# Performance work log

Measured on AMD Instinct MI355X. Metric: run time of the kernel, lower is better.

Reference implementation:

```python
import jax, jax.numpy as jnp
from jax import lax
import numpy as np

B = 16
H0 = 56
W0 = 56
C = 768
HEADS = 12
SCALES = 3
WS = 7
LC = C // SCALES          # 256 local channels per scale group
HD = C // HEADS           # 64 head dim (= conv groups)
LH = HEADS // SCALES      # 4 local heads per group


def setup_inputs() -> dict:
    key = jax.random.key(0)
    ks = jax.random.split(key, 6)
    x = jax.random.normal(ks[0], (B, H0 * W0, C), jnp.float32)
    w_qkv = jax.random.normal(ks[1], (3 * C, C), jnp.float32) * 0.02
    w_proj = jax.random.normal(ks[2], (C, C), jnp.float32) * 0.02
    b_proj = jnp.zeros((C,), jnp.float32)
    # grouped conv (groups = head_dim = 64): weight (out=LC, in_per_group=LC//HD, 3, 3)
    conv1_w = jax.random.normal(ks[3], (LC, LC // HD, 3, 3), jnp.float32) * 0.05
    conv1_b = jnp.zeros((LC,), jnp.float32)
    conv2_w = jax.random.normal(ks[4], (LC, LC // HD, 3, 3), jnp.float32) * 0.05
    conv2_b = jnp.zeros((LC,), jnp.float32)
    return {"x": x, "w_qkv": w_qkv, "w_proj": w_proj, "b_proj": b_proj,
            "conv1_w": conv1_w, "conv1_b": conv1_b,
            "conv2_w": conv2_w, "conv2_b": conv2_b,
            "H": H0, "W": W0}


def _grouped_conv(xc, w, b, stride, pad, dil):
    y = lax.conv_general_dilated(
        xc, w, window_strides=(stride, stride),
        padding=((pad, pad), (pad, pad)), rhs_dilation=(dil, dil),
        feature_group_count=HD,
        dimension_numbers=("NCHW", "OIHW", "NCHW"))
    return y + b[None, :, None, None]


def _maxpool2(xc):
    return lax.reduce_window(xc, -jnp.inf, lax.max,
                             (1, 1, 2, 2), (1, 1, 2, 2), "VALID")


def _patchify(arr):
    # arr: (B, LC, Hs, Ws) -> (B*n_region, LH, WS*WS, HD)
    b, lc, hs, ws = arr.shape
    a = arr.reshape(b, lc, hs // WS, WS, ws // WS, WS)
    a = a.transpose(0, 2, 4, 3, 5, 1).reshape(-1, WS * WS, lc)
    a = a.reshape(-1, WS * WS, LH, lc // LH).transpose(0, 2, 1, 3)
    return a


def reference(x, w_qkv, w_proj, b_proj, conv1_w, conv1_b, conv2_w, conv2_b, H, W):
    scale = HD ** -0.5
    Bx, N, Cx = x.shape
    # (B, N, 3C) -> (B, H, W, 3, C) -> (B, 3, C, H, W)
    qkv = (x @ w_qkv.T).reshape(Bx, H, W, 3, Cx).transpose(0, 3, 4, 1, 2)
    N_g = (H // WS) * (W // WS)
    conv_params = [(conv1_w, conv1_b, 1, 1, 1), (conv2_w, conv2_b, 2, 2, 2)]
    outs = []
    for i in range(SCALES):
        g = qkv[:, :, i * LC:(i + 1) * LC]  # (B, 3, LC, H, W)
        Hs, Ws = H >> i, W >> i
        if i > 0:
            w, b, st, pd, dl = conv_params[i - 1]
            g = g.reshape(Bx * 3, LC, H, W)
            g = _maxpool2(_grouped_conv(g, w, b, st, pd, dl))
            g = g.reshape(Bx, 3, LC, Hs, Ws)
        q = _patchify(g[:, 0])
        k = _patchify(g[:, 1])
        v = _patchify(g[:, 2])
        attn = jax.nn.softmax(jnp.einsum("whpd,whqd->whpq", q, k) * scale, axis=-1)
        y = jnp.einsum("whpq,whqd->whpd", attn, v)  # (B*nreg, LH, 49, HD)
        nreg = (Hs // WS) * (Ws // WS)
        y = y.reshape(Bx, nreg, LH, WS * WS, HD).transpose(0, 2, 1, 3, 4)
        if i > 0:
            y = jnp.tile(y, (1, 1, N_g // nreg, 1, 1))
        outs.append(y)
    fused = jnp.concatenate(outs, axis=1)  # (B, HEADS, N_g, 49, HD)
    fused = fused.reshape(Bx, HEADS, -1, HD).transpose(0, 2, 1, 3).reshape(Bx, N, Cx)
    return fused @ w_proj.T + b_proj
```

## Files before the change

kernel.cpp:

```cpp
#include <hip/hip_runtime.h>

typedef __attribute__((ext_vector_type(4))) float f32x4;
typedef __attribute__((ext_vector_type(8))) short bf16x8;
typedef __attribute__((ext_vector_type(4))) unsigned short u16x4;
typedef unsigned short u16;

__device__ static u16   g_xh[(size_t)50176 * 768];
__device__ static u16   g_wqkvh[(size_t)2304 * 768];
__device__ static u16   g_wprojh[(size_t)768 * 768];
__device__ static u16   g_qkv[(size_t)50176 * 2304];
__device__ static u16   g_g1[(size_t)48 * 784 * 256];
__device__ static u16   g_g2[(size_t)48 * 196 * 256];
__device__ static u16   g_fh[(size_t)50176 * 768];

static __device__ __forceinline__ u16 f2bf(float x){
  unsigned u = __float_as_uint(x);
  u += 0x7fffu + ((u >> 16) & 1u);
  return (u16)(u >> 16);
}
static __device__ __forceinline__ float bf2f(u16 h){
  return __uint_as_float(((unsigned)h) << 16);
}

__global__ __launch_bounds__(256)
void cvt_bf16_3(const float* __restrict__ i0, u16* __restrict__ o0, int n0,
                const float* __restrict__ i1, u16* __restrict__ o1, int n1,
                const float* __restrict__ i2, u16* __restrict__ o2, int n2)
{
  const int total = n0 + n1 + n2;
  int i = blockIdx.x * blockDim.x + threadIdx.x;
  const int stride = gridDim.x * blockDim.x;
  for (; i < total; i += stride) {
    const float* in; u16* out; int j = i;
    if (j < n0)           { in = i0; out = o0; }
    else if (j < n0 + n1) { in = i1; out = o1; j -= n0; }
    else                  { in = i2; out = o2; j -= n0 + n1; }
    const f32x4 v = ((const f32x4*)in)[j];
    u16x4 o;
    #pragma unroll
    for (int k = 0; k < 4; k++) o[k] = f2bf(v[k]);
    ((u16x4*)out)[j] = o;
  }
}

template<bool BIAS, typename OUT_T>
__global__ __launch_bounds__(512, 2)
void gemm256(const u16* __restrict__ A0, const u16* __restrict__ Bw,
             const float* __restrict__ bias, OUT_T* __restrict__ C,
             int N, int K, int GX)
{
  __shared__ __align__(16) char ldsb[4 * 32768];
  const int tid = threadIdx.x;
  const int lane = tid & 63;
  const int w = tid >> 6;
  const int wm = w >> 2;
  const int wn = w & 3;
  const int l15 = lane & 15, l4 = lane >> 4;

  const int nwg = gridDim.x;
  const int bid = blockIdx.x;
  const int q8 = nwg >> 3, r8 = nwg & 7;
  const int xcd = bid & 7, lid = bid >> 3;
  const int swz = (xcd < r8 ? xcd * (q8 + 1) : r8 * (q8 + 1) + (xcd - r8) * q8) + lid;
  const int bn = swz % GX;
  const int bm = swz / GX;

  const int sq = tid >> 3;
  const int sp = tid & 7;
  const int tt = sp ^ (sq & 7);
  const int sa = tt >> 2, scc = tt & 3;
  const int srow0 = sq * 2 + sa;
  const u16* a0 = A0 + (size_t)(bm * 256 + srow0) * K + scc * 8;
  const u16* a1 = A0 + (size_t)(bm * 256 + 128 + srow0) * K + scc * 8;
  const u16* b0 = Bw + (size_t)(bn * 256 + srow0) * K + scc * 8;
  const u16* b1 = Bw + (size_t)(bn * 256 + 128 + srow0) * K + scc * 8;
  const int wofs = w << 10;

  #define GLDS(srcp, ldsoff) __builtin_amdgcn_global_load_lds( \
      (__attribute__((address_space(1))) const void*)(srcp),   \
      (__attribute__((address_space(3))) void*)(ldsb + (ldsoff)), 16, 0, 0)

  auto STAGE = [&](int s) {
    const int bb = (s & 3) << 15;
    const int ko = s * 32;
    GLDS(a0 + ko, bb + wofs);
    GLDS(a1 + ko, bb + 8192 + wofs);
    GLDS(b0 + ko, bb + 16384 + wofs);
    GLDS(b1 + ko, bb + 24576 + wofs);
  };

  f32x4 acc[8][4];
  #pragma unroll
  for (int i = 0; i < 8; i++)
    #pragma unroll
    for (int j = 0; j < 4; j++) acc[i][j] = (f32x4)0.f;

  auto COMPUTE = [&](int t) {
    const char* base = ldsb + ((t & 3) << 15);
    bf16x8 bfr[4], afr[8];
    #pragma unroll
    for (int ni = 0; ni < 4; ni++) {
      const int r = wn * 64 + ni * 16 + l15;
      const int pr = r >> 1;
      const int p = (((r & 1) << 2) + l4) ^ (pr & 7);
      bfr[ni] = *(const bf16x8*)(base + 16384 + pr * 128 + p * 16);
    }
    #pragma unroll
    for (int mi = 0; mi < 8; mi++) {
      const int r = wm * 128 + mi * 16 + l15;
      const int pr = r >> 1;
      const int p = (((r & 1) << 2) + l4) ^ (pr & 7);
      afr[mi] = *(const bf16x8*)(base + pr * 128 + p * 16);
    }
    __builtin_amdgcn_s_setprio(1);
    #pragma unroll
    for (int mi = 0; mi < 8; mi++)
      #pragma unroll
      for (int ni = 0; ni < 4; ni++)
        acc[mi][ni] = __builtin_amdgcn_mfma_f32_16x16x32_bf16(afr[mi], bfr[ni], acc[mi][ni], 0, 0, 0);
    __builtin_amdgcn_s_setprio(0);
  };

  const int T = K >> 5;
  STAGE(0);
  STAGE(1);
  for (int t = 0; t < T - 2; ++t) {
    STAGE(t + 2);
    asm volatile("s_waitcnt vmcnt(8)" ::: "memory");
    __builtin_amdgcn_sched_barrier(0);
    __builtin_amdgcn_s_barrier();
    __builtin_amdgcn_sched_barrier(0);
    COMPUTE(t);
  }
  asm volatile("s_waitcnt vmcnt(4)" ::: "memory");
  __builtin_amdgcn_sched_barrier(0);
  __builtin_amdgcn_s_barrier();
  __builtin_amdgcn_sched_barrier(0);
  COMPUTE(T - 2);
  asm volatile("s_waitcnt vmcnt(0)" ::: "memory");
  __builtin_amdgcn_sched_barrier(0);
  __builtin_amdgcn_s_barrier();
  __builtin_amdgcn_sched_barrier(0);
  COMPUTE(T - 1);
  #undef GLDS

  #pragma unroll
  for (int mi = 0; mi < 8; mi++)
    #pragma unroll
    for (int ni = 0; ni < 4; ni++) {
      const int col = bn * 256 + wn * 64 + ni * 16 + l15;
      const float bv = BIAS ? bias[col] : 0.f;
      #pragma unroll
      for (int reg = 0; reg < 4; reg++) {
        const int row = bm * 256 + wm * 128 + mi * 16 + (l4 << 2) + reg;
        const float val = acc[mi][ni][reg] + bv;
        if constexpr (sizeof(OUT_T) == 2) C[(size_t)row * N + col] = (OUT_T)f2bf(val);
        else                              C[(size_t)row * N + col] = val;
      }
    }
}

__global__ __launch_bounds__(256)
void conv_all(const u16* __restrict__ qkv,
              const float* __restrict__ c1w, const float* __restrict__ c1b,
              u16* __restrict__ g1,
              const float* __restrict__ c2w, const float* __restrict__ c2b,
              u16* __restrict__ g2)
{
  __shared__ float wl[64 * 145];
  const int g = threadIdx.x;
  const int ty = threadIdx.y;
  const int tid = ty * 64 + g;
  const int bt = blockIdx.x;
  const int b = bt / 3, t = bt - b * 3;
  const bool is1 = blockIdx.y < 196;

  const float* wsrc = is1 ? c1w : c2w;
  for (int i = tid; i < 9216; i += 256) {
    const int oc = i / 36, rem = i - oc * 36;
    wl[(oc >> 2) * 145 + (oc & 3) * 36 + rem] = wsrc[i];
  }
  __syncthreads();
  const float* wg = &wl[g * 145];

  if (is1) {
    const int p = blockIdx.y * 4 + ty;
    const int y = p / 28, x = p - y * 28;

    f32x4 f[4][4];
    #pragma unroll
    for (int i = 0; i < 4; i++) {
      const int iy = 2 * y - 1 + i;
      #pragma unroll
      for (int k = 0; k < 4; k++) {
        const int ix = 2 * x - 1 + k;
        f32x4 v = (f32x4)0.f;
        if (iy >= 0 && iy < 56 && ix >= 0 && ix < 56) {
          const u16x4 in4 = *(const u16x4*)&qkv[(size_t)(b * 3136 + iy * 56 + ix) * 2304 + t * 768 + 256 + g * 4];
          v[0] = bf2f(in4[0]); v[1] = bf2f(in4[1]); v[2] = bf2f(in4[2]); v[3] = bf2f(in4[3]);
        }
        f[i][k] = v;
      }
    }

    const f32x4 bias4 = *(const f32x4*)&c1b[g * 4];
    f32x4 best;
    #pragma unroll
    for (int j = 0; j < 4; j++) best[j] = -3.4e38f;

    #pragma unroll
    for (int dy = 0; dy < 2; dy++)
      #pragma unroll
      for (int dx = 0; dx < 2; dx++) {
        f32x4 c4 = bias4;
        #pragma unroll
        for (int ky = 0; ky < 3; ky++)
          #pragma unroll
          for (int kx = 0; kx < 3; kx++) {
            const f32x4 in4 = f[dy + ky][dx + kx];
            #pragma unroll
            for (int oc = 0; oc < 4; oc++) {
              const float* wp = &wg[oc * 36 + ky * 3 + kx];
              c4[oc] += in4[0] * wp[0] + in4[1] * wp[9] + in4[2] * wp[18] + in4[3] * wp[27];
            }
          }
        #pragma unroll
        for (int j = 0; j < 4; j++) best[j] = fmaxf(best[j], c4[j]);
      }
    u16x4 o4;
    #pragma unroll
    for (int j = 0; j < 4; j++) o4[j] = f2bf(best[j]);
    *(u16x4*)&g1[((size_t)bt * 784 + p) * 256 + g * 4] = o4;
  } else {
    const int p = (blockIdx.y - 196) * 4 + ty;
    const int y = p / 14, x = p - y * 14;

    const f32x4 bias4 = *(const f32x4*)&c2b[g * 4];
    f32x4 best;
    #pragma unroll
    for (int j = 0; j < 4; j++) best[j] = -3.4e38f;

    #pragma unroll
    for (int dy = 0; dy < 2; dy++)
      #pragma unroll
      for (int dx = 0; dx < 2; dx++) {
        const int py = 2 * y + dy, px = 2 * x + dx;
        f32x4 c4 = bias4;
        #pragma unroll
        for (int ky = 0; ky < 3; ky++) {
          const int iy = py * 2 - 2 + ky * 2;
          if (iy < 0 || iy >= 56) continue;
          #pragma unroll
          for (int kx = 0; kx < 3; kx++) {
            const int ix = px * 2 - 2 + kx * 2;
            if (ix < 0 || ix >= 56) continue;
            const u16x4 in4 = *(const u16x4*)&qkv[(size_t)(b * 3136 + iy * 56 + ix) * 2304 + t * 768 + 512 + g * 4];
            const float f0 = bf2f(in4[0]), f1 = bf2f(in4[1]), f2 = bf2f(in4[2]), f3 = bf2f(in4[3]);
            #pragma unroll
            for (int oc = 0; oc < 4; oc++) {
              const float* wp = &wg[oc * 36 + ky * 3 + kx];
              c4[oc] += f0 * wp[0] + f1 * wp[9] + f2 * wp[18] + f3 * wp[27];
            }
          }
        }
        #pragma unroll
        for (int j = 0; j < 4; j++) best[j] = fmaxf(best[j], c4[j]);
      }
    u16x4 o4;
    #pragma unroll
    for (int j = 0; j < 4; j++) o4[j] = f2bf(best[j]);
    *(u16x4*)&g2[((size_t)bt * 196 + p) * 256 + g * 4] = o4;
  }
}

template<int SRC>
static __device__ __forceinline__
void attn_body(const u16* __restrict__ src, u16* __restrict__ fh,
               int side, int Hs, int head_base, int rep,
               int unit, int lane, char* vb, char* pb)
{
  const int nreg = side * side;
  const int h = unit & 3; unit >>= 2;
  const int r = unit % nreg;
  const int b = unit / nreg;
  const int hr = r / side, wr = r - hr * side;
  const int l15 = lane & 15, l4 = lane >> 4;

  auto gidx = [&](int t, int pp, int c) -> size_t {
    const int py = pp / 7, px = pp - py * 7;
    const int yy = hr * 7 + py, xx = wr * 7 + px;
    if (SRC == 0) return ((size_t)(b * 3136 + yy * 56 + xx)) * 2304 + (size_t)(t * 768 + h * 64 + c);
    else          return ((size_t)(b * 3 + t)) * ((size_t)Hs * Hs * 256) + (size_t)(yy * Hs + xx) * 256 + h * 64 + c;
  };

  for (int i = lane; i < 1024; i += 64) {
    const int q = i >> 4, dc = i & 15;
    const int qs = q > 48 ? 48 : q;
    const u16x4 v4 = *(const u16x4*)&src[gidx(2, qs, dc * 4)];
    *(u16x4*)(vb + ((q * 128 + dc * 8) ^ (((q >> 3) & 3) << 5))) = v4;
  }

  f32x4 s[4][4];
  #pragma unroll
  for (int i = 0; i < 4; i++)
    #pragma unroll
    for (int j = 0; j < 4; j++) s[i][j] = (f32x4)0.f;

  bf16x8 bk[4][2];
  #pragma unroll
  for (int ni = 0; ni < 4; ni++) {
    const int q = ni * 16 + l15;
    const int qs = q > 48 ? 48 : q;
    #pragma unroll
    for (int ks = 0; ks < 2; ks++)
      bk[ni][ks] = *(const bf16x8*)&src[gidx(1, qs, ks * 32 + l4 * 8)];
  }
  #pragma unroll
  for (int mi = 0; mi < 4; mi++) {
    const int p = mi * 16 + l15;
    const int ps = p > 48 ? 48 : p;
    const bf16x8 a0 = *(const bf16x8*)&src[gidx(0, ps, l4 * 8)];
    const bf16x8 a1 = *(const bf16x8*)&src[gidx(0, ps, 32 + l4 * 8)];
    #pragma unroll
    for (int ni = 0; ni < 4; ni++) {
      s[mi][ni] = __builtin_amdgcn_mfma_f32_16x16x32_bf16(a0, bk[ni][0], s[mi][ni], 0, 0, 0);
      s[mi][ni] = __builtin_amdgcn_mfma_f32_16x16x32_bf16(a1, bk[ni][1], s[mi][ni], 0, 0, 0);
    }
  }

  #pragma unroll
  for (int ni = 0; ni < 4; ni++) {
    const bool bad = (ni * 16 + l15) > 48;
    #pragma unroll
    for (int mi = 0; mi < 4; mi++)
      #pragma unroll
      for (int reg = 0; reg < 4; reg++)
        s[mi][ni][reg] = bad ? -1e30f : s[mi][ni][reg];
  }

  float inv[4][4];
  #pragma unroll
  for (int mi = 0; mi < 4; mi++)
    #pragma unroll
    for (int reg = 0; reg < 4; reg++) {
      float m = fmaxf(fmaxf(s[mi][0][reg], s[mi][1][reg]), fmaxf(s[mi][2][reg], s[mi][3][reg]));
      m = fmaxf(m, __shfl_xor(m, 1));
      m = fmaxf(m, __shfl_xor(m, 2));
      m = fmaxf(m, __shfl_xor(m, 4));
      m = fmaxf(m, __shfl_xor(m, 8));
      float partial = 0.f;
      #pragma unroll
      for (int ni = 0; ni < 4; ni++) {
        const float e = __expf((s[mi][ni][reg] - m) * 0.125f);
        s[mi][ni][reg] = e;
        partial += e;
      }
      partial += __shfl_xor(partial, 1);
      partial += __shfl_xor(partial, 2);
      partial += __shfl_xor(partial, 4);
      partial += __shfl_xor(partial, 8);
      inv[mi][reg] = 1.f / partial;
    }

  #pragma unroll
  for (int mi = 0; mi < 4; mi++)
    #pragma unroll
    for (int ni = 0; ni < 4; ni++)
      #pragma unroll
      for (int reg = 0; reg < 4; reg++) {
        const int row = mi * 16 + l4 * 4 + reg;
        const int col = ni * 16 + l15;
        *(u16*)(pb + ((row * 128 + col * 2) ^ ((row & 7) << 4))) = f2bf(s[mi][ni][reg]);
      }
  __syncthreads();

  f32x4 o[4][4];
  #pragma unroll
  for (int i = 0; i < 4; i++)
    #pragma unroll
    for (int j = 0; j < 4; j++) o[i][j] = (f32x4)0.f;

  #pragma unroll
  for (int ks = 0; ks < 2; ks++) {
    bf16x8 bv[4];
    #pragma unroll
    for (int ni = 0; ni < 4; ni++)
      #pragma unroll
      for (int j = 0; j < 8; j++) {
        const int q = ks * 32 + l4 * 8 + j;
        bv[ni][j] = *(const short*)(vb + ((q * 128 + (ni * 16 + l15) * 2) ^ (((q >> 3) & 3) << 5)));
      }
    #pragma unroll
    for (int mi = 0; mi < 4; mi++) {
      const int row = mi * 16 + l15;
      const bf16x8 pa = *(const bf16x8*)(pb + ((row * 128 + (ks * 4 + l4) * 16) ^ ((row & 7) << 4)));
      #pragma unroll
      for (int ni = 0; ni < 4; ni++)
        o[mi][ni] = __builtin_amdgcn_mfma_f32_16x16x32_bf16(pa, bv[ni], o[mi][ni], 0, 0, 0);
    }
  }

  const int head = head_base + h;
  #pragma unroll
  for (int mi = 0; mi < 4; mi++)
    #pragma unroll
    for (int reg = 0; reg < 4; reg++) {
      const int p = mi * 16 + l4 * 4 + reg;
      if (p >= 49) continue;
      const float iv = inv[mi][reg];
      u16 hv[4];
      #pragma unroll
      for (int ni = 0; ni < 4; ni++) hv[ni] = f2bf(o[mi][ni][reg] * iv);
      for (int m = 0; m < rep; m++) {
        const size_t ob = ((size_t)b * 3136 + (size_t)(m * nreg + r) * 49 + p) * 768 + head * 64 + l15;
        #pragma unroll
        for (int ni = 0; ni < 4; ni++) fh[ob + ni * 16] = hv[ni];
      }
    }
}

__global__ __launch_bounds__(256)
void attn_all(const u16* __restrict__ qkv, const u16* __restrict__ g1,
              const u16* __restrict__ g2, u16* __restrict__ fh)
{
  __shared__ __align__(16) u16 sV[4][64 * 64];
  __shared__ __align__(16) u16 sP[4][64 * 64];
  const int tid = threadIdx.x;
  const int lane = tid & 63;
  const int w = tid >> 6;
  char* vb = (char*)sV[w];
  char* pb = (char*)sP[w];
  const int bid = blockIdx.x;

  if (bid < 1024) {
    attn_body<0>(qkv, fh, 8, 56, 0, 1,  bid * 4 + w,          lane, vb, pb);
  } else if (bid < 1280) {
    attn_body<1>(g1,  fh, 4, 28, 4, 4,  (bid - 1024) * 4 + w, lane, vb, pb);
  } else {
    attn_body<1>(g2,  fh, 2, 14, 8, 16, (bid - 1280) * 4 + w, lane, vb, pb);
  }
}

extern "C" void kernel_launch(void* const* d_in, const int* in_sizes, int n_in,
                              void* d_out, int out_size, void* d_ws, size_t ws_size,
                              hipStream_t stream)
{
  const float* x      = (const float*)d_in[0];
  const float* w_qkv  = (const float*)d_in[1];
  const float* w_proj = (const float*)d_in[2];
  const float* b_proj = (const float*)d_in[3];
  const float* c1w    = (const float*)d_in[4];
  const float* c1b    = (const float*)d_in[5];
  const float* c2w    = (const float*)d_in[6];
  const float* c2b    = (const float*)d_in[7];
  float* out = (float*)d_out;

  u16 *xh, *wqkvh, *wprojh, *qkvb, *g1, *g2, *fh;
  hipGetSymbolAddress((void**)&xh,     HIP_SYMBOL(g_xh));
  hipGetSymbolAddress((void**)&wqkvh,  HIP_SYMBOL(g_wqkvh));
  hipGetSymbolAddress((void**)&wprojh, HIP_SYMBOL(g_wprojh));
  hipGetSymbolAddress((void**)&qkvb,   HIP_SYMBOL(g_qkv));
  hipGetSymbolAddress((void**)&g1,     HIP_SYMBOL(g_g1));
  hipGetSymbolAddress((void**)&g2,     HIP_SYMBOL(g_g2));
  hipGetSymbolAddress((void**)&fh,     HIP_SYMBOL(g_fh));

  cvt_bf16_3<<<2048, 256, 0, stream>>>(x, xh, 50176 * 768 / 4,
                                       w_qkv, wqkvh, 2304 * 768 / 4,
                                       w_proj, wprojh, 768 * 768 / 4);

  gemm256<false, u16><<<(50176 / 256) * (2304 / 256), 512, 0, stream>>>(
      xh, wqkvh, nullptr, qkvb, 2304, 768, 2304 / 256);

  conv_all<<<dim3(48, 245), dim3(64, 4), 0, stream>>>(qkvb, c1w, c1b, g1, c2w, c2b, g2);

  attn_all<<<1024 + 256 + 64, 256, 0, stream>>>(qkvb, g1, g2, fh);

  gemm256<true, float><<<(50176 / 256) * (768 / 256), 512, 0, stream>>>(
      fh, wprojh, b_proj, out, 768, 768, 768 / 256);
}
```

Measured before the change: 616.1 us.

## Restructure grouped conv to per-channel threads sliding along output rows

The grouped conv+maxpool kernel now gives each thread one output channel, keeps its 36 weights in registers instead of LDS, and has each block sweep a whole output row. A 4x4 input patch is slid horizontally so overlapping input columns are reused rather than reloaded. This removes the shared-memory weight staging and its barrier, and cuts redundant global loads. In exchange the grid is much smaller (48x42 blocks), each thread does a serial loop over the row, and the four threads sharing a group load the same input vector.

Result: slower. 633.8 us (+2.9%).

```diff
diff --git a/kernel.cpp b/kernel.cpp
--- a/kernel.cpp
+++ b/kernel.cpp
@@ -160,6 +160,81 @@
     }
 }
 
+template<int S>
+static __device__ __forceinline__
+void conv_body(const u16* __restrict__ qkv, const float* __restrict__ wsrc,
+               const float* __restrict__ bsrc, u16* __restrict__ gout,
+               int bt, int y)
+{
+  const int ch = threadIdx.x;
+  const int g = ch >> 2;
+  const int b = bt / 3, t = bt - b * 3;
+  const int chan0 = (S == 1) ? 256 : 512;
+  const int Pout = (S == 1) ? 28 : 14;
+
+  float w36[36];
+  #pragma unroll
+  for (int j = 0; j < 9; j++) {
+    const f32x4 w4 = *(const f32x4*)&wsrc[ch * 36 + j * 4];
+    w36[j * 4 + 0] = w4[0]; w36[j * 4 + 1] = w4[1];
+    w36[j * 4 + 2] = w4[2]; w36[j * 4 + 3] = w4[3];
+  }
+  const float bv = bsrc[ch];
+
+  const int rowstart = (S == 1) ? 2 * y - 1 : 4 * y - 2;
+  const size_t basech = (size_t)t * 768 + chan0 + g * 4;
+
+  auto load = [&](int iy, int ix) -> f32x4 {
+    f32x4 v = (f32x4)0.f;
+    if (iy >= 0 && iy < 56 && ix >= 0 && ix < 56) {
+      const u16x4 in4 = *(const u16x4*)&qkv[(size_t)(b * 3136 + iy * 56 + ix) * 2304 + basech];
+      v[0] = bf2f(in4[0]); v[1] = bf2f(in4[1]);
+      v[2] = bf2f(in4[2]); v[3] = bf2f(in4[3]);
+    }
+    return v;
+  };
+
+  const int c0 = (S == 1) ? -1 : -2;
+  f32x4 pat[4][4];
+  #pragma unroll
+  for (int i = 0; i < 4; i++)
+    #pragma unroll
+    for (int k = 0; k < 4; k++)
+      pat[i][k] = load(rowstart + i * S, c0 + k * S);
+
+  for (int x = 0; x < Pout; ++x) {
+    float best = -3.4e38f;
+    #pragma unroll
+    for (int dy = 0; dy < 2; dy++)
+      #pragma unroll
+      for (int dx = 0; dx < 2; dx++) {
+        float c = bv;
+        #pragma unroll
+        for (int ky = 0; ky < 3; ky++)
+          #pragma unroll
+          for (int kx = 0; kx < 3; kx++) {
+            const f32x4 in4 = pat[dy + ky][dx + kx];
+            const int tp = ky * 3 + kx;
+            c += in4[0] * w36[tp] + in4[1] * w36[9 + tp] +
+                 in4[2] * w36[18 + tp] + in4[3] * w36[27 + tp];
+          }
+        best = fmaxf(best, c);
+      }
+    gout[((size_t)bt * (Pout * Pout) + y * Pout + x) * 256 + ch] = f2bf(best);
+
+    if (x + 1 < Pout) {
+      const int nc0 = c0 + (x + 1) * 2 * S;
+      #pragma unroll
+      for (int i = 0; i < 4; i++) {
+        pat[i][0] = pat[i][2];
+        pat[i][1] = pat[i][3];
+        pat[i][2] = load(rowstart + i * S, nc0 + 2 * S);
+        pat[i][3] = load(rowstart + i * S, nc0 + 3 * S);
+      }
+    }
+  }
+}
+
 __global__ __launch_bounds__(256)
 void conv_all(const u16* __restrict__ qkv,
               const float* __restrict__ c1w, const float* __restrict__ c1b,
@@ -167,110 +242,10 @@
               const float* __restrict__ c2w, const float* __restrict__ c2b,
               u16* __restrict__ g2)
 {
-  __shared__ float wl[64 * 145];
-  const int g = threadIdx.x;
-  const int ty = threadIdx.y;
-  const int tid = ty * 64 + g;
   const int bt = blockIdx.x;
-  const int b = bt / 3, t = bt - b * 3;
-  const bool is1 = blockIdx.y < 196;
-
-  const float* wsrc = is1 ? c1w : c2w;
-  for (int i = tid; i < 9216; i += 256) {
-    const int oc = i / 36, rem = i - oc * 36;
-    wl[(oc >> 2) * 145 + (oc & 3) * 36 + rem] = wsrc[i];
-  }
-  __syncthreads();
-  const float* wg = &wl[g * 145];
-
-  if (is1) {
-    const int p = blockIdx.y * 4 + ty;
-    const int y = p / 28, x = p - y * 28;
-
-    f32x4 f[4][4];
-    #pragma unroll
-    for (int i = 0; i < 4; i++) {
-      const int iy = 2 * y - 1 + i;
-      #pragma unroll
-      for (int k = 0; k < 4; k++) {
-        const int ix = 2 * x - 1 + k;
-        f32x4 v = (f32x4)0.f;
-        if (iy >= 0 && iy < 56 && ix >= 0 && ix < 56) {
-          const u16x4 in4 = *(const u16x4*)&qkv[(size_t)(b * 3136 + iy * 56 + ix) * 2304 + t * 768 + 256 + g * 4];
-          v[0] = bf2f(in4[0]); v[1] = bf2f(in4[1]); v[2] = bf2f(in4[2]); v[3] = bf2f(in4[3]);
-        }
-        f[i][k] = v;
-      }
-    }
-
-    const f32x4 bias4 = *(const f32x4*)&c1b[g * 4];
-    f32x4 best;
-    #pragma unroll
-    for (int j = 0; j < 4; j++) best[j] = -3.4e38f;
-
-    #pragma unroll
-    for (int dy = 0; dy < 2; dy++)
-      #pragma unroll
-      for (int dx = 0; dx < 2; dx++) {
-        f32x4 c4 = bias4;
-        #pragma unroll
-        for (int ky = 0; ky < 3; ky++)
-          #pragma unroll
-          for (int kx = 0; kx < 3; kx++) {
-            const f32x4 in4 = f[dy + ky][dx + kx];
-            #pragma unroll
-            for (int oc = 0; oc < 4; oc++) {
-              const float* wp = &wg[oc * 36 + ky * 3 + kx];
-              c4[oc] += in4[0] * wp[0] + in4[1] * wp[9] + in4[2] * wp[18] + in4[3] * wp[27];
-            }
-          }
-        #pragma unroll
-        for (int j = 0; j < 4; j++) best[j] = fmaxf(best[j], c4[j]);
-      }
-    u16x4 o4;
-    #pragma unroll
-    for (int j = 0; j < 4; j++) o4[j] = f2bf(best[j]);
-    *(u16x4*)&g1[((size_t)bt * 784 + p) * 256 + g * 4] = o4;
-  } else {
-    const int p = (blockIdx.y - 196) * 4 + ty;
-    const int y = p / 14, x = p - y * 14;
-
-    const f32x4 bias4 = *(const f32x4*)&c2b[g * 4];
-    f32x4 best;
-    #pragma unroll
-    for (int j = 0; j < 4; j++) best[j] = -3.4e38f;
-
-    #pragma unroll
-    for (int dy = 0; dy < 2; dy++)
-      #pragma unroll
-      for (int dx = 0; dx < 2; dx++) {
-        const int py = 2 * y + dy, px = 2 * x + dx;
-        f32x4 c4 = bias4;
-        #pragma unroll
-        for (int ky = 0; ky < 3; ky++) {
-          const int iy = py * 2 - 2 + ky * 2;
-          if (iy < 0 || iy >= 56) continue;
-          #pragma unroll
-          for (int kx = 0; kx < 3; kx++) {
-            const int ix = px * 2 - 2 + kx * 2;
-            if (ix < 0 || ix >= 56) continue;
-            const u16x4 in4 = *(const u16x4*)&qkv[(size_t)(b * 3136 + iy * 56 + ix) * 2304 + t * 768 + 512 + g * 4];
-            const float f0 = bf2f(in4[0]), f1 = bf2f(in4[1]), f2 = bf2f(in4[2]), f3 = bf2f(in4[3]);
-            #pragma unroll
-            for (int oc = 0; oc < 4; oc++) {
-              const float* wp = &wg[oc * 36 + ky * 3 + kx];
-              c4[oc] += f0 * wp[0] + f1 * wp[9] + f2 * wp[18] + f3 * wp[27];
-            }
-          }
-        }
-        #pragma unroll
-        for (int j = 0; j < 4; j++) best[j] = fmaxf(best[j], c4[j]);
-      }
-    u16x4 o4;
-    #pragma unroll
-    for (int j = 0; j < 4; j++) o4[j] = f2bf(best[j]);
-    *(u16x4*)&g2[((size_t)bt * 196 + p) * 256 + g * 4] = o4;
-  }
+  const int yy = blockIdx.y;
+  if (yy < 28) conv_body<1>(qkv, c1w, c1b, g1, bt, yy);
+  else         conv_body<2>(qkv, c2w, c2b, g2, bt, yy - 28);
 }
 
 template<int SRC>
@@ -471,7 +446,7 @@
   gemm256<false, u16><<<(50176 / 256) * (2304 / 256), 512, 0, stream>>>(
       xh, wqkvh, nullptr, qkvb, 2304, 768, 2304 / 256);
 
-  conv_all<<<dim3(48, 245), dim3(64, 4), 0, stream>>>(qkvb, c1w, c1b, g1, c2w, c2b, g2);
+  conv_all<<<dim3(48, 42), 256, 0, stream>>>(qkvb, c1w, c1b, g1, c2w, c2b, g2);
 
   attn_all<<<1024 + 256 + 64, 256, 0, stream>>>(qkvb, g1, g2, fh);
 
```
